# Kernel tuning notes

Hardware: AMD Instinct MI355X
Metric: run time of the kernel (lower is better)

Reference implementation:

```python
import jax, jax.numpy as jnp
import numpy as np

B, S, E, NUM_CLASSES = 4, 4096, 256, 16

def setup_inputs() -> dict:
    key = jax.random.key(0)
    ks = jax.random.split(key, 10)
    std = E ** -0.5
    return {
        "x":  jax.random.normal(ks[0], (B, S, E), dtype=jnp.float32),
        "wq": jax.random.normal(ks[1], (E, E), dtype=jnp.float32) * std,
        "bq": jnp.zeros((E,), dtype=jnp.float32),
        "wk": jax.random.normal(ks[2], (E, E), dtype=jnp.float32) * std,
        "bk": jnp.zeros((E,), dtype=jnp.float32),
        "wv": jax.random.normal(ks[3], (E, E), dtype=jnp.float32) * std,
        "bv": jnp.zeros((E,), dtype=jnp.float32),
        "wo": jax.random.normal(ks[4], (NUM_CLASSES, E), dtype=jnp.float32) * std,
        "bo": jnp.zeros((NUM_CLASSES,), dtype=jnp.float32),
    }

def reference(x, wq, bq, wk, bk, wv, bv, wo, bo):
    embed_dim = wq.shape[0]
    scaling = embed_dim ** -0.5  # float(embed_dim) ** (-0.5)
    # torch Linear: y = x @ W.T + b
    Q = jnp.einsum('bse,oe->bso', x, wq) + bq
    K = jnp.einsum('bse,oe->bso', x, wk) + bk
    V = jnp.einsum('bse,oe->bso', x, wv) + bv
    # scores: [B, S, S]
    scores = jnp.einsum('bqe,bke->bqk', Q, K) * scaling
    # original code has `/ (embed_dim ^ 0.5)`; intended math is / sqrt(embed_dim)
    attn = jax.nn.softmax(scores, axis=-1) * scaling
    attn_out = jnp.einsum('bqk,bke->bqe', attn, V)
    return jnp.einsum('bqe,oe->bqo', attn_out, wo) + bo
```

## Files before the change

kernel.cpp:

```cpp
#include <hip/hip_runtime.h>
#include <hip/hip_bf16.h>


#define S_ 4096
#define E_ 256
#define B_ 4
#define NC_ 16
#define BS_ (B_ * S_)
#define NS_ 4

typedef __attribute__((ext_vector_type(8))) short bf16x8;
typedef __attribute__((ext_vector_type(4))) float f32x4;

__device__ __forceinline__ unsigned short bf16_rtne(float f) {
    unsigned int u = __float_as_uint(f);
    return (unsigned short)((u + 0x7FFFu + ((u >> 16) & 1u)) >> 16);
}
__device__ __forceinline__ bf16x8 pack8(f32x4 a, f32x4 b) {
    bf16x8 r;
#pragma unroll
    for (int i = 0; i < 4; i++) r[i] = (short)bf16_rtne(a[i]);
#pragma unroll
    for (int i = 0; i < 4; i++) r[4 + i] = (short)bf16_rtne(b[i]);
    return r;
}
__device__ __forceinline__ void gl_lds16(const void* g, void* lds) {
    __builtin_amdgcn_global_load_lds(
        (const __attribute__((address_space(1))) unsigned int*)g,
        (__attribute__((address_space(3))) unsigned int*)lds, 16, 0, 0);
}

__global__ __launch_bounds__(256) void qkv_gemm(
    const float* __restrict__ x, const float* __restrict__ wq,
    const float* __restrict__ wk, const float* __restrict__ wv,
    const float* __restrict__ bq, const float* __restrict__ bk,
    const float* __restrict__ bv, short* __restrict__ Qb,
    short* __restrict__ Kb, short* __restrict__ Vtc) {
    __shared__ bf16x8 xt[256];
    __shared__ bf16x8 wt[1024];
    __shared__ short epi[16896];

    int t = threadIdx.x;
    int sel = blockIdx.x, m0 = blockIdx.y * 64;
    int lane = t & 63, wid = t >> 6, quad = lane >> 4, idx = lane & 15;

    const float* w = (sel == 0) ? wq : (sel == 1) ? wk : wv;
    const float* bias = (sel == 0) ? bq : (sel == 1) ? bk : bv;

    const float* xsrc = x + (size_t)(m0 + (t >> 2)) * E_ + (t & 3) * 8;

    f32x4 zf = {0.f, 0.f, 0.f, 0.f};
    f32x4 acc[16];
#pragma unroll
    for (int i = 0; i < 16; i++) acc[i] = zf;

    for (int kc = 0; kc < E_; kc += 32) {
        f32x4 a0 = *(const f32x4*)(xsrc + kc);
        f32x4 a1 = *(const f32x4*)(xsrc + kc + 4);
        xt[t] = pack8(a0, a1);
#pragma unroll
        for (int i = 0; i < 4; i++) {
            int p = i * 256 + t;
            const float* ws = w + (size_t)(p >> 2) * E_ + (p & 3) * 8 + kc;
            f32x4 b0 = *(const f32x4*)ws;
            f32x4 b1 = *(const f32x4*)(ws + 4);
            wt[p] = pack8(b0, b1);
        }
        __syncthreads();
        bf16x8 af = xt[(wid * 16 + idx) * 4 + quad];
#pragma unroll
        for (int ct = 0; ct < 16; ct++)
            acc[ct] = __builtin_amdgcn_mfma_f32_16x16x32_bf16(
                af, wt[(ct * 16 + idx) * 4 + quad], acc[ct], 0, 0, 0);
        __syncthreads();
    }

    int qr = quad * 4;
    if (sel == 2) {
#pragma unroll
        for (int ct = 0; ct < 16; ct++) {
            int e = ct * 16 + idx;
            float bb = bias[e];
#pragma unroll
            for (int r = 0; r < 4; r++) {
                int mr = wid * 16 + qr + r;
                int ckg = mr >> 5, sin = mr & 31;
                int sp = ((sin & 15) << 1) | (sin >> 4);
                int pos = (sp >> 3) ^ ((e >> 1) & 3);
                epi[ckg * 8192 + e * 32 + pos * 8 + (sp & 7)] =
                    (short)bf16_rtne(acc[ct][r] + bb);
            }
        }
        __syncthreads();
        size_t base = ((size_t)((m0 >> 12) * 128 + ((m0 & (S_ - 1)) >> 5))) * 8192;
#pragma unroll
        for (int j = 0; j < 8; j++) {
            int unit = j * 256 + t;
            *(bf16x8*)(Vtc + base + (size_t)unit * 8) = *(const bf16x8*)&epi[unit * 8];
        }
    } else {
        float alpha = (sel == 0) ? 0.0625f : 1.0f;
#pragma unroll
        for (int ct = 0; ct < 16; ct++) {
            int n = ct * 16 + idx;
            float bb = bias[n];
#pragma unroll
            for (int r = 0; r < 4; r++) {
                int row = wid * 16 + qr + r;
                int col = (sel == 1) ? ((((n >> 3) ^ (row & 7)) << 3) | (n & 7)) : n;
                epi[row * 264 + col] = (short)bf16_rtne((acc[ct][r] + bb) * alpha);
            }
        }
        __syncthreads();
        short* out = (sel == 0) ? Qb : Kb;
#pragma unroll
        for (int j = 0; j < 8; j++) {
            int g = j * 256 + t;
            int row = g >> 5, seg = g & 31;
            *(bf16x8*)(out + (size_t)(m0 + row) * E_ + seg * 8) =
                *(const bf16x8*)&epi[row * 264 + seg * 8];
        }
    }
}

__global__ __launch_bounds__(256, 2) void flash_attn(
    const short* __restrict__ Qb, const short* __restrict__ Kb,
    const short* __restrict__ Vtc, short* __restrict__ Opart,
    float* __restrict__ lpart) {
    __shared__ __align__(16) short lds[36864];

    int t = threadIdx.x;
    int b = blockIdx.z, slice = blockIdx.y, q0 = blockIdx.x * 128;
    int key0 = slice * (S_ / NS_);
    const int nchunk = (S_ / NS_) / 32;
    int lane = t & 63, wv = t >> 6, quad = lane >> 4, idx = lane & 15;

    bf16x8 qf[2][8];
#pragma unroll
    for (int u = 0; u < 2; u++) {
        const short* qrow = Qb + (size_t)(b * S_ + q0 + u * 64 + wv * 16 + idx) * E_ + quad * 8;
#pragma unroll
        for (int c = 0; c < 8; c++) qf[u][c] = *(const bf16x8*)(qrow + c * 32);
    }

    f32x4 zf = {0.f, 0.f, 0.f, 0.f};
    f32x4 oacc[2][16];
#pragma unroll
    for (int u = 0; u < 2; u++)
#pragma unroll
        for (int i = 0; i < 16; i++) oacc[u][i] = zf;
    float ls[2][4] = {{0, 0, 0, 0}, {0, 0, 0, 0}};

    const short* kg = Kb + (size_t)(b * S_ + key0) * E_ + lane * 8;
    const short* vg = Vtc + ((size_t)(b * 128 + (key0 >> 5))) * 8192 + lane * 8;
    short* psw = lds + 32768 + wv * 1024;
    unsigned int* pswu = (unsigned int*)psw;
    int vsw = (quad ^ ((idx >> 1) & 3)) << 3;

#pragma unroll
    for (int j = 0; j < 4; j++) gl_lds16(kg + (wv * 4 + j) * 512, &lds[(wv * 4 + j) * 512]);
#pragma unroll
    for (int j = 0; j < 4; j++) gl_lds16(vg + (wv * 4 + j) * 512, &lds[16384 + (wv * 4 + j) * 512]);
#pragma unroll
    for (int j = 0; j < 4; j++) gl_lds16(kg + 8192 + (wv * 4 + j) * 512, &lds[8192 + (wv * 4 + j) * 512]);
    __syncthreads();

    {
        f32x4 s[4] = {zf, zf, zf, zf};
#pragma unroll
        for (int c = 0; c < 8; c++) {
            int p = (((c * 4 + quad) ^ (idx & 7)) << 3);
            bf16x8 k0 = *(const bf16x8*)&lds[idx * 256 + p];
            bf16x8 k1 = *(const bf16x8*)&lds[(16 + idx) * 256 + p];
            s[0] = __builtin_amdgcn_mfma_f32_16x16x32_bf16(qf[0][c], k0, s[0], 0, 0, 0);
            s[1] = __builtin_amdgcn_mfma_f32_16x16x32_bf16(qf[0][c], k1, s[1], 0, 0, 0);
            s[2] = __builtin_amdgcn_mfma_f32_16x16x32_bf16(qf[1][c], k0, s[2], 0, 0, 0);
            s[3] = __builtin_amdgcn_mfma_f32_16x16x32_bf16(qf[1][c], k1, s[3], 0, 0, 0);
        }
#pragma unroll
        for (int u = 0; u < 2; u++)
#pragma unroll
            for (int r = 0; r < 4; r++) {
                float p0 = __expf(s[u * 2][r]);
                float p1 = __expf(s[u * 2 + 1][r]);
                ls[u][r] += p0 + p1;
                pswu[u * 256 + (quad * 4 + r) * 16 + idx] =
                    (unsigned int)bf16_rtne(p0) | ((unsigned int)bf16_rtne(p1) << 16);
            }
    }

    for (int ck = 0; ck < nchunk - 1; ck++) {
        __syncthreads();
        if (ck + 2 < nchunk) {
            const short* ks = kg + (size_t)(ck + 2) * 8192;
            short* kd = lds + (ck & 1) * 8192;
#pragma unroll
            for (int j = 0; j < 4; j++) gl_lds16(ks + (wv * 4 + j) * 512, &kd[(wv * 4 + j) * 512]);
        }
        {
            const short* vs = vg + (size_t)(ck + 1) * 8192;
            short* vd = lds + 16384 + ((ck + 1) & 1) * 8192;
#pragma unroll
            for (int j = 0; j < 4; j++) gl_lds16(vs + (wv * 4 + j) * 512, &vd[(wv * 4 + j) * 512]);
        }
        const short* kc = lds + ((ck + 1) & 1) * 8192;
        f32x4 s[4] = {zf, zf, zf, zf};
#pragma unroll
        for (int c = 0; c < 8; c++) {
            int p = (((c * 4 + quad) ^ (idx & 7)) << 3);
            bf16x8 k0 = *(const bf16x8*)&kc[idx * 256 + p];
            bf16x8 k1 = *(const bf16x8*)&kc[(16 + idx) * 256 + p];
            s[0] = __builtin_amdgcn_mfma_f32_16x16x32_bf16(qf[0][c], k0, s[0], 0, 0, 0);
            s[1] = __builtin_amdgcn_mfma_f32_16x16x32_bf16(qf[0][c], k1, s[1], 0, 0, 0);
            s[2] = __builtin_amdgcn_mfma_f32_16x16x32_bf16(qf[1][c], k0, s[2], 0, 0, 0);
            s[3] = __builtin_amdgcn_mfma_f32_16x16x32_bf16(qf[1][c], k1, s[3], 0, 0, 0);
        }
        bf16x8 af0 = *(const bf16x8*)&psw[idx * 32 + quad * 8];
        bf16x8 af1 = *(const bf16x8*)&psw[512 + idx * 32 + quad * 8];
#pragma unroll
        for (int u = 0; u < 2; u++)
#pragma unroll
            for (int r = 0; r < 4; r++) {
                float p0 = __expf(s[u * 2][r]);
                float p1 = __expf(s[u * 2 + 1][r]);
                ls[u][r] += p0 + p1;
                pswu[u * 256 + (quad * 4 + r) * 16 + idx] =
                    (unsigned int)bf16_rtne(p0) | ((unsigned int)bf16_rtne(p1) << 16);
            }
        const short* vc = lds + 16384 + (ck & 1) * 8192;
#pragma unroll
        for (int ct = 0; ct < 16; ct++) {
            bf16x8 v = *(const bf16x8*)&vc[(ct * 16 + idx) * 32 + vsw];
            oacc[0][ct] = __builtin_amdgcn_mfma_f32_16x16x32_bf16(af0, v, oacc[0][ct], 0, 0, 0);
            oacc[1][ct] = __builtin_amdgcn_mfma_f32_16x16x32_bf16(af1, v, oacc[1][ct], 0, 0, 0);
        }
    }
    __syncthreads();
    {
        bf16x8 af0 = *(const bf16x8*)&psw[idx * 32 + quad * 8];
        bf16x8 af1 = *(const bf16x8*)&psw[512 + idx * 32 + quad * 8];
        const short* vc = lds + 16384 + ((nchunk - 1) & 1) * 8192;
#pragma unroll
        for (int ct = 0; ct < 16; ct++) {
            bf16x8 v = *(const bf16x8*)&vc[(ct * 16 + idx) * 32 + vsw];
            oacc[0][ct] = __builtin_amdgcn_mfma_f32_16x16x32_bf16(af0, v, oacc[0][ct], 0, 0, 0);
            oacc[1][ct] = __builtin_amdgcn_mfma_f32_16x16x32_bf16(af1, v, oacc[1][ct], 0, 0, 0);
        }
    }
    __syncthreads();

#pragma unroll
    for (int u = 0; u < 2; u++)
#pragma unroll
        for (int r = 0; r < 4; r++) {
            float v = ls[u][r];
            v += __shfl_xor(v, 1);
            v += __shfl_xor(v, 2);
            v += __shfl_xor(v, 4);
            v += __shfl_xor(v, 8);
            if (idx == 0)
                lpart[(size_t)slice * BS_ + b * S_ + q0 + u * 64 + wv * 16 + quad * 4 + r] = v;
        }

    short* scr = lds + wv * 8192;
#pragma unroll
    for (int u = 0; u < 2; u++)
#pragma unroll
        for (int ct = 0; ct < 16; ct++) {
            int e = ct * 16 + idx;
#pragma unroll
            for (int r = 0; r < 4; r++) {
                int lr = quad * 4 + r;
                scr[u * 4096 + lr * 256 + ((((e >> 3) ^ (lr & 7)) << 3) | (e & 7))] =
                    (short)bf16_rtne(oacc[u][ct][r]);
            }
        }
#pragma unroll
    for (int u = 0; u < 2; u++) {
        size_t obase = ((size_t)slice * BS_ + (size_t)b * S_ + q0 + u * 64 + wv * 16) * E_;
#pragma unroll
        for (int j = 0; j < 8; j++) {
            int unit = j * 64 + lane;
            *(bf16x8*)(Opart + obase + (size_t)unit * 8) =
                *(const bf16x8*)&scr[u * 4096 + unit * 8];
        }
    }
}

__global__ __launch_bounds__(256) void proj_out(
    const short* __restrict__ Opart, const float* __restrict__ lpart,
    const float* __restrict__ wo, const float* __restrict__ bo,
    float* __restrict__ out) {
    __shared__ __align__(16) short at2[2][16384];
    int t = threadIdx.x;
    int m0 = blockIdx.x * 64;
    int lane = t & 63, wv = t >> 6, quad = lane >> 4, idx = lane & 15;

    bf16x8 bw[8];
#pragma unroll
    for (int c = 0; c < 8; c++) {
        const float* ws = wo + idx * E_ + c * 32 + quad * 8;
        f32x4 w0 = *(const f32x4*)ws;
        f32x4 w1 = *(const f32x4*)(ws + 4);
        bw[c] = pack8(w0, w1);
    }

#pragma unroll
    for (int j = 0; j < 8; j++)
        gl_lds16(Opart + (size_t)m0 * E_ + (wv * 8 + j) * 512 + lane * 8,
                 &at2[0][(wv * 8 + j) * 512]);

    f32x4 acc = {0.f, 0.f, 0.f, 0.f};
    for (int ns = 0; ns < NS_; ns++) {
        __syncthreads();
        if (ns + 1 < NS_) {
            const short* src = Opart + ((size_t)(ns + 1) * BS_ + m0) * E_ + lane * 8;
#pragma unroll
            for (int j = 0; j < 8; j++)
                gl_lds16(src + (wv * 8 + j) * 512, &at2[(ns + 1) & 1][(wv * 8 + j) * 512]);
        }
        const short* a = at2[ns & 1];
#pragma unroll
        for (int c = 0; c < 8; c++) {
            bf16x8 af = *(const bf16x8*)&a[(wv * 16 + idx) * 256 +
                                           ((((c * 4 + quad) ^ (idx & 7)) << 3))];
            acc = __builtin_amdgcn_mfma_f32_16x16x32_bf16(af, bw[c], acc, 0, 0, 0);
        }
    }
#pragma unroll
    for (int r = 0; r < 4; r++) {
        int m = m0 + wv * 16 + quad * 4 + r;
        float ltot = 0.f;
#pragma unroll
        for (int ns = 0; ns < NS_; ns++) ltot += lpart[(size_t)ns * BS_ + m];
        out[(size_t)m * NC_ + idx] = acc[r] * (0.0625f / ltot) + bo[idx];
    }
}

extern "C" void kernel_launch(void* const* d_in, const int* in_sizes, int n_in,
                              void* d_out, int out_size, void* d_ws, size_t ws_size,
                              hipStream_t stream) {
    const float* x  = (const float*)d_in[0];
    const float* wq = (const float*)d_in[1];
    const float* bq = (const float*)d_in[2];
    const float* wk = (const float*)d_in[3];
    const float* bk = (const float*)d_in[4];
    const float* wv = (const float*)d_in[5];
    const float* bv = (const float*)d_in[6];
    const float* wo = (const float*)d_in[7];
    const float* bo = (const float*)d_in[8];
    float* out = (float*)d_out;

    const size_t NEL = (size_t)BS_ * E_;
    short* Qb = (short*)d_ws;
    short* Kb = Qb + NEL;
    short* Vtc = Kb + NEL;
    short* Opart = Vtc + NEL;
    float* lpart = (float*)(Opart + (size_t)NS_ * NEL);

    qkv_gemm<<<dim3(3, BS_ / 64), 256, 0, stream>>>(x, wq, wk, wv, bq, bk, bv, Qb, Kb, Vtc);
    flash_attn<<<dim3(S_ / 128, NS_, B_), 256, 0, stream>>>(Qb, Kb, Vtc, Opart, lpart);
    proj_out<<<BS_ / 64, 256, 0, stream>>>(Opart, lpart, wo, bo, out);
}
```

Baseline: 179.9 us.

## Load V fragments directly from global into registers instead of staging in LDS

The V tile is no longer staged through LDS with async global-to-LDS copies. Each lane now reads its MFMA B-operand fragments straight from global memory, using a small rolling register window interleaved with the PV MFMAs. The V layout written by the projection kernel drops its swizzle, and the P scratch is double-buffered so one barrier per chunk is enough. LDS drops from 72KB to 48KB, which may allow more blocks per CU, but the V reads now expose global/L2 latency inside the inner loop.

```diff
diff --git a/kernel.cpp b/kernel.cpp
--- a/kernel.cpp
+++ b/kernel.cpp
@@ -86,9 +86,7 @@
                 int mr = wid * 16 + qr + r;
                 int ckg = mr >> 5, sin = mr & 31;
                 int sp = ((sin & 15) << 1) | (sin >> 4);
-                int pos = (sp >> 3) ^ ((e >> 1) & 3);
-                epi[ckg * 8192 + e * 32 + pos * 8 + (sp & 7)] =
-                    (short)bf16_rtne(acc[ct][r] + bb);
+                epi[ckg * 8192 + e * 32 + sp] = (short)bf16_rtne(acc[ct][r] + bb);
             }
         }
         __syncthreads();
@@ -127,7 +125,7 @@
     const short* __restrict__ Qb, const short* __restrict__ Kb,
     const short* __restrict__ Vtc, short* __restrict__ Opart,
     float* __restrict__ lpart) {
-    __shared__ __align__(16) short lds[36864];
+    __shared__ __align__(16) short lds[24576];
 
     int t = threadIdx.x;
     int b = blockIdx.z, slice = blockIdx.y, q0 = blockIdx.x * 128;
@@ -152,15 +150,10 @@
     float ls[2][4] = {{0, 0, 0, 0}, {0, 0, 0, 0}};
 
     const short* kg = Kb + (size_t)(b * S_ + key0) * E_ + lane * 8;
-    const short* vg = Vtc + ((size_t)(b * 128 + (key0 >> 5))) * 8192 + lane * 8;
-    short* psw = lds + 32768 + wv * 1024;
-    unsigned int* pswu = (unsigned int*)psw;
-    int vsw = (quad ^ ((idx >> 1) & 3)) << 3;
+    const short* vp = Vtc + ((size_t)(b * 128 + (key0 >> 5))) * 8192 + idx * 32 + quad * 8;
 
 #pragma unroll
     for (int j = 0; j < 4; j++) gl_lds16(kg + (wv * 4 + j) * 512, &lds[(wv * 4 + j) * 512]);
-#pragma unroll
-    for (int j = 0; j < 4; j++) gl_lds16(vg + (wv * 4 + j) * 512, &lds[16384 + (wv * 4 + j) * 512]);
 #pragma unroll
     for (int j = 0; j < 4; j++) gl_lds16(kg + 8192 + (wv * 4 + j) * 512, &lds[8192 + (wv * 4 + j) * 512]);
     __syncthreads();
@@ -177,16 +170,18 @@
             s[2] = __builtin_amdgcn_mfma_f32_16x16x32_bf16(qf[1][c], k0, s[2], 0, 0, 0);
             s[3] = __builtin_amdgcn_mfma_f32_16x16x32_bf16(qf[1][c], k1, s[3], 0, 0, 0);
         }
-#pragma unroll
-        for (int u = 0; u < 2; u++)
-#pragma unroll
-            for (int r = 0; r < 4; r++) {
-                float p0 = __expf(s[u * 2][r]);
-                float p1 = __expf(s[u * 2 + 1][r]);
-                ls[u][r] += p0 + p1;
-                pswu[u * 256 + (quad * 4 + r) * 16 + idx] =
-                    (unsigned int)bf16_rtne(p0) | ((unsigned int)bf16_rtne(p1) << 16);
-            }
+        unsigned int* pw = (unsigned int*)(lds + 16384 + wv * 1024);
+#pragma unroll
+        for (int r = 0; r < 4; r++) {
+            float a0 = __expf(s[0][r]), a1 = __expf(s[1][r]);
+            float b0 = __expf(s[2][r]), b1 = __expf(s[3][r]);
+            ls[0][r] += a0 + a1;
+            ls[1][r] += b0 + b1;
+            pw[(quad * 4 + r) * 16 + idx] =
+                (unsigned int)bf16_rtne(a0) | ((unsigned int)bf16_rtne(a1) << 16);
+            pw[256 + (quad * 4 + r) * 16 + idx] =
+                (unsigned int)bf16_rtne(b0) | ((unsigned int)bf16_rtne(b1) << 16);
+        }
     }
 
     for (int ck = 0; ck < nchunk - 1; ck++) {
@@ -197,12 +192,11 @@
 #pragma unroll
             for (int j = 0; j < 4; j++) gl_lds16(ks + (wv * 4 + j) * 512, &kd[(wv * 4 + j) * 512]);
         }
-        {
-            const short* vs = vg + (size_t)(ck + 1) * 8192;
-            short* vd = lds + 16384 + ((ck + 1) & 1) * 8192;
-#pragma unroll
-            for (int j = 0; j < 4; j++) gl_lds16(vs + (wv * 4 + j) * 512, &vd[(wv * 4 + j) * 512]);
-        }
+        const short* vq = vp + (size_t)ck * 8192;
+        bf16x8 vwin[4];
+#pragma unroll
+        for (int j = 0; j < 4; j++) vwin[j] = *(const bf16x8*)(vq + j * 512);
+
         const short* kc = lds + ((ck + 1) & 1) * 8192;
         f32x4 s[4] = {zf, zf, zf, zf};
 #pragma unroll
@@ -215,34 +209,39 @@
             s[2] = __builtin_amdgcn_mfma_f32_16x16x32_bf16(qf[1][c], k0, s[2], 0, 0, 0);
             s[3] = __builtin_amdgcn_mfma_f32_16x16x32_bf16(qf[1][c], k1, s[3], 0, 0, 0);
         }
-        bf16x8 af0 = *(const bf16x8*)&psw[idx * 32 + quad * 8];
-        bf16x8 af1 = *(const bf16x8*)&psw[512 + idx * 32 + quad * 8];
-#pragma unroll
-        for (int u = 0; u < 2; u++)
-#pragma unroll
-            for (int r = 0; r < 4; r++) {
-                float p0 = __expf(s[u * 2][r]);
-                float p1 = __expf(s[u * 2 + 1][r]);
-                ls[u][r] += p0 + p1;
-                pswu[u * 256 + (quad * 4 + r) * 16 + idx] =
-                    (unsigned int)bf16_rtne(p0) | ((unsigned int)bf16_rtne(p1) << 16);
+        const short* psp = lds + 16384 + (ck & 1) * 4096 + wv * 1024;
+        bf16x8 af0 = *(const bf16x8*)&psp[idx * 32 + quad * 8];
+        bf16x8 af1 = *(const bf16x8*)&psp[512 + idx * 32 + quad * 8];
+        unsigned int* pw = (unsigned int*)(lds + 16384 + ((ck + 1) & 1) * 4096 + wv * 1024);
+#pragma unroll
+        for (int g = 0; g < 4; g++) {
+            float a0 = __expf(s[0][g]), a1 = __expf(s[1][g]);
+            float b0 = __expf(s[2][g]), b1 = __expf(s[3][g]);
+            ls[0][g] += a0 + a1;
+            ls[1][g] += b0 + b1;
+            pw[(quad * 4 + g) * 16 + idx] =
+                (unsigned int)bf16_rtne(a0) | ((unsigned int)bf16_rtne(a1) << 16);
+            pw[256 + (quad * 4 + g) * 16 + idx] =
+                (unsigned int)bf16_rtne(b0) | ((unsigned int)bf16_rtne(b1) << 16);
+#pragma unroll
+            for (int cc = 0; cc < 4; cc++) {
+                int ct = g * 4 + cc;
+                bf16x8 v = vwin[cc];
+                if (ct + 4 < 16) vwin[cc] = *(const bf16x8*)(vq + (ct + 4) * 512);
+                oacc[0][ct] = __builtin_amdgcn_mfma_f32_16x16x32_bf16(af0, v, oacc[0][ct], 0, 0, 0);
+                oacc[1][ct] = __builtin_amdgcn_mfma_f32_16x16x32_bf16(af1, v, oacc[1][ct], 0, 0, 0);
             }
-        const short* vc = lds + 16384 + (ck & 1) * 8192;
+        }
+    }
+    {
+        int ck = nchunk - 1;
+        const short* vq = vp + (size_t)ck * 8192;
+        const short* psp = lds + 16384 + (ck & 1) * 4096 + wv * 1024;
+        bf16x8 af0 = *(const bf16x8*)&psp[idx * 32 + quad * 8];
+        bf16x8 af1 = *(const bf16x8*)&psp[512 + idx * 32 + quad * 8];
 #pragma unroll
         for (int ct = 0; ct < 16; ct++) {
-            bf16x8 v = *(const bf16x8*)&vc[(ct * 16 + idx) * 32 + vsw];
-            oacc[0][ct] = __builtin_amdgcn_mfma_f32_16x16x32_bf16(af0, v, oacc[0][ct], 0, 0, 0);
-            oacc[1][ct] = __builtin_amdgcn_mfma_f32_16x16x32_bf16(af1, v, oacc[1][ct], 0, 0, 0);
-        }
-    }
-    __syncthreads();
-    {
-        bf16x8 af0 = *(const bf16x8*)&psw[idx * 32 + quad * 8];
-        bf16x8 af1 = *(const bf16x8*)&psw[512 + idx * 32 + quad * 8];
-        const short* vc = lds + 16384 + ((nchunk - 1) & 1) * 8192;
-#pragma unroll
-        for (int ct = 0; ct < 16; ct++) {
-            bf16x8 v = *(const bf16x8*)&vc[(ct * 16 + idx) * 32 + vsw];
+            bf16x8 v = *(const bf16x8*)(vq + ct * 512);
             oacc[0][ct] = __builtin_amdgcn_mfma_f32_16x16x32_bf16(af0, v, oacc[0][ct], 0, 0, 0);
             oacc[1][ct] = __builtin_amdgcn_mfma_f32_16x16x32_bf16(af1, v, oacc[1][ct], 0, 0, 0);
         }
@@ -262,27 +261,24 @@
                 lpart[(size_t)slice * BS_ + b * S_ + q0 + u * 64 + wv * 16 + quad * 4 + r] = v;
         }
 
-    short* scr = lds + wv * 8192;
-#pragma unroll
-    for (int u = 0; u < 2; u++)
+    short* scr = lds + wv * 4096;
+#pragma unroll
+    for (int u = 0; u < 2; u++) {
 #pragma unroll
         for (int ct = 0; ct < 16; ct++) {
             int e = ct * 16 + idx;
 #pragma unroll
             for (int r = 0; r < 4; r++) {
                 int lr = quad * 4 + r;
-                scr[u * 4096 + lr * 256 + ((((e >> 3) ^ (lr & 7)) << 3) | (e & 7))] =
+                scr[lr * 256 + ((((e >> 3) ^ (lr & 7)) << 3) | (e & 7))] =
                     (short)bf16_rtne(oacc[u][ct][r]);
             }
         }
-#pragma unroll
-    for (int u = 0; u < 2; u++) {
         size_t obase = ((size_t)slice * BS_ + (size_t)b * S_ + q0 + u * 64 + wv * 16) * E_;
 #pragma unroll
         for (int j = 0; j < 8; j++) {
             int unit = j * 64 + lane;
-            *(bf16x8*)(Opart + obase + (size_t)unit * 8) =
-                *(const bf16x8*)&scr[u * 4096 + unit * 8];
+            *(bf16x8*)(Opart + obase + (size_t)unit * 8) = *(const bf16x8*)&scr[unit * 8];
         }
     }
 }
```

Result: slower. 286.0 us (+58.9%).
